# Kernel tuning notes

Hardware: AMD Instinct MI355X
Metric: run time of the kernel (lower is better)

Reference implementation:

```python
import jax, jax.numpy as jnp
import numpy as np

B, VOCAB, F = 4096, 50000, 64


def setup_inputs() -> dict:
    key = jax.random.key(0)
    k1, k2 = jax.random.split(key, 2)
    # binary multi-hot input (row > 0 mask semantics of the original)
    x = jax.random.randint(k1, (B, VOCAB), 0, 2, dtype=jnp.int32)
    # truncated-normal-ish init for the factor embedding table
    V = (jax.random.normal(k2, (VOCAB, F), dtype=jnp.float32) * 0.05)
    # linear (first-order) bias table is zero-initialized in the original
    bias = jnp.zeros((VOCAB, 1), dtype=jnp.float32)
    g_bias = jnp.zeros((), dtype=jnp.float32)
    return {"x": x, "V": V, "bias": bias, "g_bias": g_bias}


def reference(x, V, bias, g_bias):
    # x: [B, VOCAB] binary multi-hot; V: [VOCAB, F]; bias: [VOCAB, 1]; g_bias: scalar
    xf = x.astype(V.dtype)
    # FM sum-square identity: for selected rows S = {i : x_i > 0},
    # 0.5 * (sum_{i,j in S} <v_i, v_j> - sum_{i in S} ||v_i||^2)
    #   = 0.5 * (||sum_i v_i||^2 - sum_i ||v_i||^2)
    xv = xf @ V                                   # [B, F] = sum of selected rows
    sum_sq = jnp.sum(xv * xv, axis=-1)            # [B]
    sq_sum = xf @ jnp.sum(V * V, axis=-1)         # [B]
    second_order = 0.5 * (sum_sq - sq_sum)        # [B]
    linear = g_bias + xf @ bias                   # [B, 1]
    return linear + second_order[:, None]         # [B, 1]
```

## Files before the change

### kernel.cpp

```cpp
#include <hip/hip_runtime.h>

#define VOCAB 50000
#define BROWS 4096
#define F 64
#define NCOLS 80
#define NT 5
#define SPLITS 16
#define NR 98
#define KT_TOTAL (SPLITS * NR)
#define KPAD (KT_TOTAL * 32)

#define AS1 __attribute__((address_space(1)))
#define AS3 __attribute__((address_space(3)))

typedef __attribute__((ext_vector_type(4))) float f32x4;
typedef __attribute__((ext_vector_type(8))) short s16x8;

__device__ __forceinline__ unsigned short f2bf(float f) {
    unsigned u = __builtin_bit_cast(unsigned, f);
    unsigned r = (u + 0x7FFFu + ((u >> 16) & 1u)) >> 16;
    return (unsigned short)r;
}
__device__ __forceinline__ float bf2f(unsigned short b) {
    unsigned u = ((unsigned)b) << 16;
    return __builtin_bit_cast(float, u);
}

__global__ void fm_prep_w(const float* __restrict__ V, const float* __restrict__ bias,
                          float* __restrict__ w) {
    int k = blockIdx.x * blockDim.x + threadIdx.x;
    if (k >= KPAD) return;
    float val = 0.f;
    if (k < VOCAB) {
        const float4* row = reinterpret_cast<const float4*>(V + (size_t)k * F);
        float ss = 0.f;
#pragma unroll
        for (int j = 0; j < F / 4; ++j) {
            float4 v = row[j];
            ss += v.x * v.x + v.y * v.y + v.z * v.z + v.w * v.w;
        }
        val = bias[k] - 0.5f * ss;
    }
    w[k] = val;
}

__global__ void fm_prep_bfrag(const float* __restrict__ V, const float* __restrict__ w,
                              uint4* __restrict__ bfrag) {
    int t = blockIdx.x * blockDim.x + threadIdx.x;
    if (t >= KT_TOTAL * NT * 64) return;
    int lane = t & 63;
    int tile = t >> 6;
    int nt = tile % NT;
    int kt = tile / NT;
    int n = nt * 16 + (lane & 15);
    int kbase = kt * 32 + (lane >> 4) * 8;
    unsigned short o[8];
#pragma unroll
    for (int j = 0; j < 8; ++j) {
        int k = kbase + j;
        float v = 0.f;
        if (k < VOCAB) {
            if (n < F) {
                v = V[(size_t)k * F + n];
            } else if (n == F) {
                v = w[k];
            } else if (n == F + 1) {
                float wv = w[k];
                v = wv - bf2f(f2bf(wv));
            }
        }
        o[j] = f2bf(v);
    }
    uint4 pk;
    pk.x = (unsigned)o[0] | ((unsigned)o[1] << 16);
    pk.y = (unsigned)o[2] | ((unsigned)o[3] << 16);
    pk.z = (unsigned)o[4] | ((unsigned)o[5] << 16);
    pk.w = (unsigned)o[6] | ((unsigned)o[7] << 16);
    bfrag[t] = pk;
}

__global__ __launch_bounds__(256, 4) void fm_main(const int* __restrict__ x,
                                                  const uint4* __restrict__ bfrag,
                                                  float* __restrict__ part) {
    __shared__ uint4 bbuf[2][NT * 64];
    const int bx = blockIdx.x;
    const int split = bx & (SPLITS - 1);
    const int mblock = bx >> 4;
    const int tid = threadIdx.x;
    const int wave = tid >> 6;
    const int lane = tid & 63;
    const int kb = lane >> 4;
    const int rowA = mblock * 64 + wave * 16 + (lane & 15);
    const int* __restrict__ xrow = x + (size_t)rowA * VOCAB;
    const int kt0 = split * NR;
    const int e0 = (wave << 6) + lane;

    auto stage = [&](int rnd) {
        const uint4* src = bfrag + (size_t)(kt0 + rnd) * (NT * 64);
        uint4* dst = bbuf[rnd & 1];
        __builtin_amdgcn_global_load_lds((const AS1 void*)(src + e0),
                                         (AS3 void*)(dst + (wave << 6)), 16, 0, 0);
        if (wave == 0)
            __builtin_amdgcn_global_load_lds((const AS1 void*)(src + 256 + lane),
                                             (AS3 void*)(dst + 256), 16, 0, 0);
    };
    auto batchload = [&](int r0, int4* d) {
#pragma unroll
        for (int j = 0; j < 4; ++j) {
            const int r = r0 + j;
            if (r >= NR) continue;
            const int k = (kt0 + r) * 32 + kb * 8;
            if ((kt0 + r) * 32 + 32 <= VOCAB) {
                d[2 * j]     = *reinterpret_cast<const int4*>(xrow + k);
                d[2 * j + 1] = *reinterpret_cast<const int4*>(xrow + k + 4);
            } else {
                int v[8];
#pragma unroll
                for (int jj = 0; jj < 8; ++jj) v[jj] = (k + jj < VOCAB) ? xrow[k + jj] : 0;
                d[2 * j]     = make_int4(v[0], v[1], v[2], v[3]);
                d[2 * j + 1] = make_int4(v[4], v[5], v[6], v[7]);
            }
        }
    };
    auto mk = [&](int4 a0, int4 a1) -> s16x8 {
        uint4 apk;
        apk.x = ((unsigned)a0.x + ((unsigned)a0.y << 16)) * 16256u;
        apk.y = ((unsigned)a0.z + ((unsigned)a0.w << 16)) * 16256u;
        apk.z = ((unsigned)a1.x + ((unsigned)a1.y << 16)) * 16256u;
        apk.w = ((unsigned)a1.z + ((unsigned)a1.w << 16)) * 16256u;
        return __builtin_bit_cast(s16x8, apk);
    };

    f32x4 acc[NT];
#pragma unroll
    for (int nt = 0; nt < NT; ++nt) acc[nt] = (f32x4){0.f, 0.f, 0.f, 0.f};

    auto roundbody = [&](int r, int4 a0, int4 a1) {
        if (r + 1 < NR) stage(r + 1);
        s16x8 af = mk(a0, a1);
        const uint4* bb = bbuf[r & 1];
#pragma unroll
        for (int nt = 0; nt < NT; ++nt) {
            s16x8 bf = __builtin_bit_cast(s16x8, bb[nt * 64 + lane]);
            acc[nt] = __builtin_amdgcn_mfma_f32_16x16x32_bf16(af, bf, acc[nt], 0, 0, 0);
        }
        __syncthreads();
    };

    int4 xcur[8], xnxt[8];
    stage(0);
    batchload(0, xcur);
    __syncthreads();

    for (int s = 0; s < 12; ++s) {
        const int r0 = 8 * s;
        batchload(r0 + 4, xnxt);
        roundbody(r0 + 0, xcur[0], xcur[1]);
        roundbody(r0 + 1, xcur[2], xcur[3]);
        roundbody(r0 + 2, xcur[4], xcur[5]);
        roundbody(r0 + 3, xcur[6], xcur[7]);
        batchload(r0 + 8, xcur);
        roundbody(r0 + 4, xnxt[0], xnxt[1]);
        roundbody(r0 + 5, xnxt[2], xnxt[3]);
        roundbody(r0 + 6, xnxt[4], xnxt[5]);
        roundbody(r0 + 7, xnxt[6], xnxt[7]);
    }
    roundbody(96, xcur[0], xcur[1]);
    roundbody(97, xcur[2], xcur[3]);

    float* __restrict__ p = part + (size_t)split * BROWS * NCOLS;
    int m0 = mblock * 64 + wave * 16 + kb * 4;
    int c0 = lane & 15;
#pragma unroll
    for (int nt = 0; nt < NT; ++nt)
#pragma unroll
        for (int r = 0; r < 4; ++r)
            p[(size_t)(m0 + r) * NCOLS + nt * 16 + c0] = acc[nt][r];
}

__global__ void fm_reduce(const float* __restrict__ part, const float* __restrict__ gbias,
                          float* __restrict__ out) {
    int b = blockIdx.x * 4 + (threadIdx.x >> 6);
    int lane = threadIdx.x & 63;
    float acc = 0.f;
#pragma unroll
    for (int s = 0; s < SPLITS; ++s)
        acc += part[((size_t)s * BROWS + b) * NCOLS + lane];
    float sq = acc * acc;
    float ex = 0.f;
    if (lane < 16)       ex = part[((size_t)lane * BROWS + b) * NCOLS + F];
    else if (lane < 32)  ex = part[((size_t)(lane - 16) * BROWS + b) * NCOLS + F + 1];
#pragma unroll
    for (int off = 32; off; off >>= 1) {
        sq += __shfl_xor(sq, off, 64);
        ex += __shfl_xor(ex, off, 64);
    }
    if (lane == 0) out[b] = gbias[0] + ex + 0.5f * sq;
}

extern "C" void kernel_launch(void* const* d_in, const int* in_sizes, int n_in,
                              void* d_out, int out_size, void* d_ws, size_t ws_size,
                              hipStream_t stream) {
    const int*   x     = (const int*)d_in[0];
    const float* V     = (const float*)d_in[1];
    const float* bias  = (const float*)d_in[2];
    const float* gbias = (const float*)d_in[3];
    float* out = (float*)d_out;

    char* ws = (char*)d_ws;
    uint4* bfrag = (uint4*)ws;
    float* w     = (float*)(ws + (size_t)KT_TOTAL * NT * 64 * 16);
    float* part  = (float*)(ws + (size_t)KT_TOTAL * NT * 64 * 16 + (size_t)KPAD * 4);

    fm_prep_w<<<(KPAD + 255) / 256, 256, 0, stream>>>(V, bias, w);
    fm_prep_bfrag<<<(KT_TOTAL * NT * 64 + 255) / 256, 256, 0, stream>>>(V, w, bfrag);
    fm_main<<<(BROWS / 64) * SPLITS, 256, 0, stream>>>(x, bfrag, part);
    fm_reduce<<<BROWS / 4, 256, 0, stream>>>(part, gbias, out);
}
```

Baseline: 208.1 us.

## Pack multi-hot input into bitmask before the MFMA main kernel

Adds a pre-pass that compresses the int32 multi-hot matrix into one bit per entry, and changes the main kernel to read one byte per lane per k-tile and expand it into bf16 ones and zeros. The main loop is simplified to a single rolled loop with one-step prefetch of the mask byte. Total traffic over the large input is unchanged, since the pack kernel still streams all of x once. What it removes is the strided, register-heavy int4 loads inside the MFMA kernel. In exchange it adds an extra kernel launch and a bitmask workspace, and the main loop now issues small byte loads with less latency hiding.

```diff
diff --git a/kernel.cpp b/kernel.cpp
--- a/kernel.cpp
+++ b/kernel.cpp
@@ -9,6 +9,8 @@
 #define NR 98
 #define KT_TOTAL (SPLITS * NR)
 #define KPAD (KT_TOTAL * 32)
+#define RDWORDS (KPAD / 32)
+#define RBYTES  (KPAD / 8)
 
 #define AS1 __attribute__((address_space(1)))
 #define AS3 __attribute__((address_space(3)))
@@ -24,6 +26,29 @@
 __device__ __forceinline__ float bf2f(unsigned short b) {
     unsigned u = ((unsigned)b) << 16;
     return __builtin_bit_cast(float, u);
+}
+
+__global__ void fm_pack(const int* __restrict__ x, unsigned* __restrict__ xb) {
+    const int T = blockIdx.x * 256 + threadIdx.x;
+    const int b = T / RDWORDS;
+    const int t = T - b * RDWORDS;
+    const int k0 = t * 32;
+    const int* xr = x + (size_t)b * VOCAB + k0;
+    unsigned bits = 0;
+    if (k0 + 32 <= VOCAB) {
+        const int4* p = reinterpret_cast<const int4*>(xr);
+#pragma unroll
+        for (int q = 0; q < 8; ++q) {
+            int4 v = p[q];
+            bits |= (unsigned)(v.x & 1) << (4 * q);
+            bits |= (unsigned)(v.y & 1) << (4 * q + 1);
+            bits |= (unsigned)(v.z & 1) << (4 * q + 2);
+            bits |= (unsigned)(v.w & 1) << (4 * q + 3);
+        }
+    } else if (k0 < VOCAB) {
+        for (int j = 0; j < VOCAB - k0; ++j) bits |= (unsigned)(xr[j] & 1) << j;
+    }
+    xb[(size_t)b * RDWORDS + t] = bits;
 }
 
 __global__ void fm_prep_w(const float* __restrict__ V, const float* __restrict__ bias,
@@ -79,7 +104,7 @@
     bfrag[t] = pk;
 }
 
-__global__ __launch_bounds__(256, 4) void fm_main(const int* __restrict__ x,
+__global__ __launch_bounds__(256, 4) void fm_main(const unsigned char* __restrict__ xb,
                                                   const uint4* __restrict__ bfrag,
                                                   float* __restrict__ part) {
     __shared__ uint4 bbuf[2][NT * 64];
@@ -91,8 +116,8 @@
     const int lane = tid & 63;
     const int kb = lane >> 4;
     const int rowA = mblock * 64 + wave * 16 + (lane & 15);
-    const int* __restrict__ xrow = x + (size_t)rowA * VOCAB;
     const int kt0 = split * NR;
+    const unsigned char* __restrict__ xp = xb + (size_t)rowA * RBYTES + kb + (size_t)kt0 * 4;
     const int e0 = (wave << 6) + lane;
 
     auto stage = [&](int rnd) {
@@ -104,30 +129,12 @@
             __builtin_amdgcn_global_load_lds((const AS1 void*)(src + 256 + lane),
                                              (AS3 void*)(dst + 256), 16, 0, 0);
     };
-    auto batchload = [&](int r0, int4* d) {
-#pragma unroll
-        for (int j = 0; j < 4; ++j) {
-            const int r = r0 + j;
-            if (r >= NR) continue;
-            const int k = (kt0 + r) * 32 + kb * 8;
-            if ((kt0 + r) * 32 + 32 <= VOCAB) {
-                d[2 * j]     = *reinterpret_cast<const int4*>(xrow + k);
-                d[2 * j + 1] = *reinterpret_cast<const int4*>(xrow + k + 4);
-            } else {
-                int v[8];
-#pragma unroll
-                for (int jj = 0; jj < 8; ++jj) v[jj] = (k + jj < VOCAB) ? xrow[k + jj] : 0;
-                d[2 * j]     = make_int4(v[0], v[1], v[2], v[3]);
-                d[2 * j + 1] = make_int4(v[4], v[5], v[6], v[7]);
-            }
-        }
-    };
-    auto mk = [&](int4 a0, int4 a1) -> s16x8 {
+    auto unpack = [&](unsigned m) -> s16x8 {
         uint4 apk;
-        apk.x = ((unsigned)a0.x + ((unsigned)a0.y << 16)) * 16256u;
-        apk.y = ((unsigned)a0.z + ((unsigned)a0.w << 16)) * 16256u;
-        apk.z = ((unsigned)a1.x + ((unsigned)a1.y << 16)) * 16256u;
-        apk.w = ((unsigned)a1.z + ((unsigned)a1.w << 16)) * 16256u;
+        apk.x = ((m & 1u)   ? 0x3F80u : 0u) | ((m & 2u)   ? 0x3F800000u : 0u);
+        apk.y = ((m & 4u)   ? 0x3F80u : 0u) | ((m & 8u)   ? 0x3F800000u : 0u);
+        apk.z = ((m & 16u)  ? 0x3F80u : 0u) | ((m & 32u)  ? 0x3F800000u : 0u);
+        apk.w = ((m & 64u)  ? 0x3F80u : 0u) | ((m & 128u) ? 0x3F800000u : 0u);
         return __builtin_bit_cast(s16x8, apk);
     };
 
@@ -135,9 +142,17 @@
 #pragma unroll
     for (int nt = 0; nt < NT; ++nt) acc[nt] = (f32x4){0.f, 0.f, 0.f, 0.f};
 
-    auto roundbody = [&](int r, int4 a0, int4 a1) {
-        if (r + 1 < NR) stage(r + 1);
-        s16x8 af = mk(a0, a1);
+    stage(0);
+    unsigned cb = xp[0];
+    __syncthreads();
+
+    for (int r = 0; r < NR; ++r) {
+        unsigned nb = 0;
+        if (r + 1 < NR) {
+            stage(r + 1);
+            nb = xp[(r + 1) * 4];
+        }
+        s16x8 af = unpack(cb);
         const uint4* bb = bbuf[r & 1];
 #pragma unroll
         for (int nt = 0; nt < NT; ++nt) {
@@ -145,28 +160,8 @@
             acc[nt] = __builtin_amdgcn_mfma_f32_16x16x32_bf16(af, bf, acc[nt], 0, 0, 0);
         }
         __syncthreads();
-    };
-
-    int4 xcur[8], xnxt[8];
-    stage(0);
-    batchload(0, xcur);
-    __syncthreads();
-
-    for (int s = 0; s < 12; ++s) {
-        const int r0 = 8 * s;
-        batchload(r0 + 4, xnxt);
-        roundbody(r0 + 0, xcur[0], xcur[1]);
-        roundbody(r0 + 1, xcur[2], xcur[3]);
-        roundbody(r0 + 2, xcur[4], xcur[5]);
-        roundbody(r0 + 3, xcur[6], xcur[7]);
-        batchload(r0 + 8, xcur);
-        roundbody(r0 + 4, xnxt[0], xnxt[1]);
-        roundbody(r0 + 5, xnxt[2], xnxt[3]);
-        roundbody(r0 + 6, xnxt[4], xnxt[5]);
-        roundbody(r0 + 7, xnxt[6], xnxt[7]);
-    }
-    roundbody(96, xcur[0], xcur[1]);
-    roundbody(97, xcur[2], xcur[3]);
+        cb = nb;
+    }
 
     float* __restrict__ p = part + (size_t)split * BROWS * NCOLS;
     int m0 = mblock * 64 + wave * 16 + kb * 4;
@@ -208,12 +203,15 @@
     float* out = (float*)d_out;
 
     char* ws = (char*)d_ws;
-    uint4* bfrag = (uint4*)ws;
-    float* w     = (float*)(ws + (size_t)KT_TOTAL * NT * 64 * 16);
-    float* part  = (float*)(ws + (size_t)KT_TOTAL * NT * 64 * 16 + (size_t)KPAD * 4);
-
+    unsigned* xbw  = (unsigned*)ws;
+    uint4* bfrag   = (uint4*)(ws + (size_t)BROWS * RBYTES);
+    float* w       = (float*)(ws + (size_t)BROWS * RBYTES + (size_t)KT_TOTAL * NT * 64 * 16);
+    float* part    = (float*)(ws + (size_t)BROWS * RBYTES + (size_t)KT_TOTAL * NT * 64 * 16
+                              + (size_t)KPAD * 4);
+
+    fm_pack<<<(BROWS * RDWORDS) / 256, 256, 0, stream>>>(x, xbw);
     fm_prep_w<<<(KPAD + 255) / 256, 256, 0, stream>>>(V, bias, w);
     fm_prep_bfrag<<<(KT_TOTAL * NT * 64 + 255) / 256, 256, 0, stream>>>(V, w, bfrag);
-    fm_main<<<(BROWS / 64) * SPLITS, 256, 0, stream>>>(x, bfrag, part);
+    fm_main<<<(BROWS / 64) * SPLITS, 256, 0, stream>>>((const unsigned char*)xbw, bfrag, part);
     fm_reduce<<<BROWS / 4, 256, 0, stream>>>(part, gbias, out);
 }
```

Result: slower. 245.8 us (+18.1%).
